# Optimization experiments

Hardware: AMD Instinct MI355X
Metric: run time of the kernel (lower is better)

The kernel has to match this reference:

```python
import jax, jax.numpy as jnp
import numpy as np
import math

B, S, D, H = 4, 2048, 1024, 16
DH = D // H  # 64
DFF = 4 * D
EPS = 1e-5


def layer_norm(x, g, b):
    mu = jnp.mean(x, axis=-1, keepdims=True)
    var = jnp.mean(jnp.square(x - mu), axis=-1, keepdims=True)
    return (x - mu) * jax.lax.rsqrt(var + EPS) * g + b


def apply_rope(xq, xk, freqs_cis):
    # xq, xk: [B, S, H, DH]; freqs_cis: [S, DH//2, 2] (cos, sin)
    cos = freqs_cis[None, :, None, :, 0]  # [1, S, 1, DH//2]
    sin = freqs_cis[None, :, None, :, 1]

    def rot(t):
        tr = t.reshape(*t.shape[:-1], DH // 2, 2)
        t0, t1 = tr[..., 0], tr[..., 1]
        o0 = t0 * cos - t1 * sin
        o1 = t0 * sin + t1 * cos
        return jnp.stack([o0, o1], axis=-1).reshape(t.shape)

    return rot(xq), rot(xk)


def setup_inputs() -> dict:
    key = jax.random.key(0)
    ks = jax.random.split(key, 12)
    x = jax.random.normal(ks[0], (B, S, D), dtype=jnp.float32)
    # rotary frequencies (theta = 10000), stored as (cos, sin)
    inv = 1.0 / (10000.0 ** (np.arange(0, DH, 2, dtype=np.float32) / DH))
    t = np.arange(S, dtype=np.float32)
    ang = np.outer(t, inv)  # [S, DH//2]
    freqs_cis = jnp.asarray(np.stack([np.cos(ang), np.sin(ang)], axis=-1))
    s = 1.0 / math.sqrt(D)
    sf = 1.0 / math.sqrt(DFF)
    return {
        "x": x,
        "freqs_cis": freqs_cis,
        "wq": jax.random.normal(ks[1], (D, D), dtype=jnp.float32) * s,
        "wk": jax.random.normal(ks[2], (D, D), dtype=jnp.float32) * s,
        "wv": jax.random.normal(ks[3], (D, D), dtype=jnp.float32) * s,
        "w_proj": jax.random.normal(ks[4], (D, D), dtype=jnp.float32) * s,
        "b_proj": jnp.zeros((D,), dtype=jnp.float32),
        "w_ff1": jax.random.normal(ks[5], (D, DFF), dtype=jnp.float32) * s,
        "b_ff1": jnp.zeros((DFF,), dtype=jnp.float32),
        "w_ff2": jax.random.normal(ks[6], (DFF, D), dtype=jnp.float32) * sf,
        "b_ff2": jnp.zeros((D,), dtype=jnp.float32),
        "ln1_g": jnp.ones((D,), dtype=jnp.float32),
        "ln1_b": jnp.zeros((D,), dtype=jnp.float32),
        "ln2_g": jnp.ones((D,), dtype=jnp.float32),
        "ln2_b": jnp.zeros((D,), dtype=jnp.float32),
    }


def reference(x, freqs_cis, wq, wk, wv, w_proj, b_proj, w_ff1, b_ff1, w_ff2,
              b_ff2, ln1_g, ln1_b, ln2_g, ln2_b):
    # --- attention block (pre-norm) ---
    h = layer_norm(x, ln1_g, ln1_b)
    xq = (h @ wq).reshape(B, S, H, DH)
    xk = (h @ wk).reshape(B, S, H, DH)
    xv = (h @ wv).reshape(B, S, H, DH)
    xq, xk = apply_rope(xq, xk, freqs_cis)
    # [B, H, S, S]
    att = jnp.einsum("bqhd,bkhd->bhqk", xq, xk) / math.sqrt(DH)
    att = jax.nn.softmax(att, axis=-1)
    out = jnp.einsum("bhqk,bkhd->bqhd", att, xv).reshape(B, S, D)
    x = x + out @ w_proj + b_proj
    # --- feed-forward block (pre-norm, GELU) ---
    h2 = layer_norm(x, ln2_g, ln2_b)
    ff = jax.nn.gelu(h2 @ w_ff1 + b_ff1, approximate=False) @ w_ff2 + b_ff2
    return x + ff
```

## Files before the change

kernel.cpp:

```cpp
#include <hip/hip_runtime.h>
#include <hip/hip_bf16.h>


#define Bb_ 4
#define Ss_ 2048
#define Dd_ 1024
#define Hh_ 16
#define DFF_ 4096

typedef __bf16 bf16x8 __attribute__((ext_vector_type(8)));
typedef float f32x4 __attribute__((ext_vector_type(4)));

static __device__ __forceinline__ unsigned short f2bf(float f) {
  union { float f; unsigned u; } v; v.f = f;
  unsigned r = v.u + 0x7FFF + ((v.u >> 16) & 1);
  return (unsigned short)(r >> 16);
}
static __device__ __forceinline__ float bf2f(unsigned short h) {
  union { unsigned u; float f; } v; v.u = ((unsigned)h) << 16;
  return v.f;
}
static __device__ __forceinline__ unsigned cvt_pk_bf16(float lo, float hi) {
  unsigned r;
  asm("v_cvt_pk_bf16_f32 %0, %1, %2" : "=v"(r) : "v"(lo), "v"(hi));
  return r;
}

static __device__ __forceinline__ void gl16(const unsigned short* g, void* l) {
  __builtin_amdgcn_global_load_lds(
      (const __attribute__((address_space(1))) void*)g,
      (__attribute__((address_space(3))) void*)l, 16, 0, 0);
}

__global__ __launch_bounds__(256) void ln_kernel(
    const float* __restrict__ x, const float* __restrict__ g,
    const float* __restrict__ bb, unsigned short* __restrict__ out)
{
  const int row = blockIdx.x;
  const int t = threadIdx.x;
  const float4 v = reinterpret_cast<const float4*>(x + (size_t)row * Dd_)[t];
  float s = v.x + v.y + v.z + v.w;
  float ss = v.x*v.x + v.y*v.y + v.z*v.z + v.w*v.w;
  #pragma unroll
  for (int o = 32; o; o >>= 1) { s += __shfl_down(s, o); ss += __shfl_down(ss, o); }
  __shared__ float red[8];
  if ((t & 63) == 0) { red[t >> 6] = s; red[4 + (t >> 6)] = ss; }
  __syncthreads();
  s = red[0] + red[1] + red[2] + red[3];
  ss = red[4] + red[5] + red[6] + red[7];
  const float mean = s * (1.f / Dd_);
  const float var = ss * (1.f / Dd_) - mean * mean;
  const float inv = rsqrtf(var + 1e-5f);
  const float4 gv = reinterpret_cast<const float4*>(g)[t];
  const float4 bv = reinterpret_cast<const float4*>(bb)[t];
  ushort4 o4;
  o4.x = f2bf((v.x - mean) * inv * gv.x + bv.x);
  o4.y = f2bf((v.y - mean) * inv * gv.y + bv.y);
  o4.z = f2bf((v.z - mean) * inv * gv.z + bv.z);
  o4.w = f2bf((v.w - mean) * inv * gv.w + bv.w);
  reinterpret_cast<ushort4*>(out + (size_t)row * Dd_)[t] = o4;
}

__global__ __launch_bounds__(256) void tconv_kernel(
    const float* __restrict__ src, unsigned short* __restrict__ dst, int K, int N)
{
  __shared__ float tile[32][33];
  const int bx = blockIdx.x, by = blockIdx.y;
  const int tx = threadIdx.x & 31, ty = threadIdx.x >> 5;
  #pragma unroll
  for (int i = 0; i < 4; i++)
    tile[ty + i * 8][tx] = src[(size_t)(by * 32 + ty + i * 8) * N + bx * 32 + tx];
  __syncthreads();
  #pragma unroll
  for (int i = 0; i < 4; i++)
    dst[(size_t)(bx * 32 + ty + i * 8) * K + by * 32 + tx] = f2bf(tile[tx][ty + i * 8]);
}

__global__ __launch_bounds__(256) void tconv3_kernel(
    const float* __restrict__ s0, const float* __restrict__ s1,
    const float* __restrict__ s2, unsigned short* __restrict__ dst)
{
  __shared__ float tile[32][33];
  const int bx = blockIdx.x, by = blockIdx.y, bz = blockIdx.z;
  const float* src = (bz == 0) ? s0 : (bz == 1) ? s1 : s2;
  unsigned short* d = dst + (size_t)bz * 1024 * 1024;
  const int tx = threadIdx.x & 31, ty = threadIdx.x >> 5;
  #pragma unroll
  for (int i = 0; i < 4; i++)
    tile[ty + i * 8][tx] = src[(size_t)(by * 32 + ty + i * 8) * 1024 + bx * 32 + tx];
  __syncthreads();
  #pragma unroll
  for (int i = 0; i < 4; i++)
    d[(size_t)(bx * 32 + ty + i * 8) * 1024 + by * 32 + tx] = f2bf(tile[tx][ty + i * 8]);
}

template<int MODE>
__global__ __launch_bounds__(256) void gemm_kernel(
    const unsigned short* __restrict__ A,
    const unsigned short* __restrict__ BT,
    int K, int nbn, int N,
    const float* __restrict__ bias,
    const float* __restrict__ resid,
    void* __restrict__ out,
    const float* __restrict__ fcp,
    void* __restrict__ out2)
{
  __shared__ unsigned short As[2][128 * 64];
  __shared__ unsigned short Bs[2][128 * 64];
  const int t = threadIdx.x;

  const int nwg = gridDim.x;
  const int id = blockIdx.x;
  const int sid = (id & 7) * (nwg >> 3) + (id >> 3);
  const int bm = sid / nbn, bn = sid % nbn;

  const int w = t >> 6, lane = t & 63;
  const int lq = lane >> 4, lr = lane & 15;
  const int wm = (w >> 1) * 64, wn = (w & 1) * 64;
  const int srow = t >> 3, sg8 = t & 7;
  const int sw8 = sg8 ^ (srow & 7);

  const unsigned short* ag = A  + (size_t)(bm * 128 + srow) * K + sw8 * 8;
  const unsigned short* bg = BT + (size_t)(bn * 128 + srow) * K + sw8 * 8;

  char* AsB = (char*)As;
  char* BsB = (char*)Bs;
  const int csw = (lr & 7) * 8;
  int aoffB[2], boffB[2];
  aoffB[0] = (wm + lr) * 128 + 2 * ((lq * 8) ^ csw);
  aoffB[1] = (wm + lr) * 128 + 2 * ((32 + lq * 8) ^ csw);
  boffB[0] = (wn + lr) * 128 + 2 * ((lq * 8) ^ csw);
  boffB[1] = (wn + lr) * 128 + 2 * ((32 + lq * 8) ^ csw);
  const int sdstB = (srow * 64 + sg8 * 8) * 2;

  f32x4 acc[4][4] = {};
  const int nt = K >> 6;

#define STAGE7(BUF)                                                          \
  {                                                                          \
    _Pragma("unroll")                                                        \
    for (int i_ = 0; i_ < 4; i_++) {                                         \
      gl16(ag + (size_t)i_ * 32 * K, AsB + (BUF) * 16384 + sdstB + i_ * 4096); \
      gl16(bg + (size_t)i_ * 32 * K, BsB + (BUF) * 16384 + sdstB + i_ * 4096); \
    }                                                                        \
    ag += 64; bg += 64;                                                      \
  }

#define COMPUTE7(BUF)                                                        \
  {                                                                          \
    __builtin_amdgcn_s_setprio(1);                                           \
    _Pragma("unroll")                                                        \
    for (int kc_ = 0; kc_ < 2; kc_++) {                                      \
      bf16x8 af[4], bfr[4];                                                  \
      _Pragma("unroll")                                                      \
      for (int i_ = 0; i_ < 4; i_++) {                                       \
        af[i_]  = *reinterpret_cast<const bf16x8*>(AsB + (BUF) * 16384 + aoffB[kc_] + i_ * 2048); \
        bfr[i_] = *reinterpret_cast<const bf16x8*>(BsB + (BUF) * 16384 + boffB[kc_] + i_ * 2048); \
      }                                                                      \
      _Pragma("unroll")                                                      \
      for (int i_ = 0; i_ < 4; i_++)                                         \
        _Pragma("unroll")                                                    \
        for (int j_ = 0; j_ < 4; j_++)                                       \
          acc[i_][j_] = __builtin_amdgcn_mfma_f32_16x16x32_bf16(af[i_], bfr[j_], acc[i_][j_], 0, 0, 0); \
    }                                                                        \
    __builtin_amdgcn_s_setprio(0);                                           \
  }

  STAGE7(0);
  __syncthreads();
  for (int t0 = 0; t0 < nt; t0 += 2) {
    STAGE7(1);
    COMPUTE7(0);
    __syncthreads();
    if (t0 + 2 < nt) STAGE7(0);
    COMPUTE7(1);
    __syncthreads();
  }
#undef STAGE7
#undef COMPUTE7

  const int growbase = bm * 128 + wm + lq * 4;
  const int gcolbase = bn * 128 + wn + lr;

  if (MODE == 0) {
    if (bn < 16) {
      const float qs = (bn < 8) ? 0.125f * 1.44269504088896f : 1.f;
      const float sgn = (lr & 1) ? 1.f : -1.f;
      #pragma unroll
      for (int j = 0; j < 4; j++) {
        const int col = gcolbase + j * 16;
        const int ip = (col & 63) & ~1;
        #pragma unroll
        for (int i = 0; i < 4; i++) {
          #pragma unroll
          for (int r = 0; r < 4; r++) {
            const int grow = growbase + i * 16 + r;
            const int s = grow & (Ss_ - 1);
            const float2 cs = *reinterpret_cast<const float2*>(fcp + (size_t)s * 64 + ip);
            const float v = acc[i][j][r];
            const float p = __shfl_xor(v, 1);
            const float o = (v * cs.x + sgn * p * cs.y) * qs;
            ((unsigned short*)out)[(size_t)grow * N + col] = f2bf(o);
          }
        }
      }
    } else {
      #pragma unroll
      for (int j = 0; j < 4; j++) {
        const int vcol = gcolbase + j * 16 - 2048;
        const int h = vcol >> 6, d = vcol & 63;
        #pragma unroll
        for (int i = 0; i < 4; i++) {
          const int g0 = growbase + i * 16;
          const int b = g0 >> 11, s0 = g0 & (Ss_ - 1);
          ushort4 o4;
          o4.x = f2bf(acc[i][j][0]);
          o4.y = f2bf(acc[i][j][1]);
          o4.z = f2bf(acc[i][j][2]);
          o4.w = f2bf(acc[i][j][3]);
          unsigned short* vr = (unsigned short*)out2 +
              ((size_t)((b * 16 + h) * 64 + d)) * Ss_ + s0;
          *reinterpret_cast<ushort4*>(vr) = o4;
        }
      }
    }
  } else {
    #pragma unroll
    for (int j = 0; j < 4; j++) {
      const int col = gcolbase + j * 16;
      const float bj = bias[col];
      #pragma unroll
      for (int i = 0; i < 4; i++) {
        #pragma unroll
        for (int r = 0; r < 4; r++) {
          const int grow = growbase + i * 16 + r;
          const float v = acc[i][j][r];
          if (MODE == 1 || MODE == 3) {
            ((float*)out)[(size_t)grow * N + col] = v + bj + resid[(size_t)grow * N + col];
          } else {
            const float u = v + bj;
            const float gel = 0.5f * u * (1.f + erff(u * 0.70710678118654752f));
            ((unsigned short*)out)[(size_t)grow * N + col] = f2bf(gel);
          }
        }
      }
    }
  }
}

__global__ __launch_bounds__(512) void attn_kernel(
    const unsigned short* __restrict__ qkv,
    const unsigned short* __restrict__ vt,
    unsigned short* __restrict__ attout)
{
  __shared__ unsigned short Ks[2][64 * 64];
  __shared__ unsigned short Vs[2][64 * 64];
  __shared__ unsigned short Ps[256 * 64];
  const int qt = blockIdx.x, h = blockIdx.y, b = blockIdx.z;
  const int t = threadIdx.x, w = t >> 6, lane = t & 63;
  const int lq = lane >> 4, lr = lane & 15;
  const int srow = t >> 3, sg8 = t & 7;

  const unsigned short* kg = qkv + (size_t)(b * Ss_) * 3072 + 1024 + h * 64;
  const unsigned short* vg = vt + (size_t)((b * 16 + h) * 64) * Ss_;

  bf16x8 aq[2][2];
  {
    const unsigned short* qg = qkv + (size_t)(b * Ss_ + qt * 256) * 3072 + h * 64;
    #pragma unroll
    for (int mt = 0; mt < 2; mt++)
      #pragma unroll
      for (int kc = 0; kc < 2; kc++)
        aq[mt][kc] = *reinterpret_cast<const bf16x8*>(
            qg + (size_t)(w * 32 + mt * 16 + lr) * 3072 + kc * 32 + lq * 8);
  }

  bf16x8 ones;
  #pragma unroll
  for (int j = 0; j < 8; j++) ones[j] = (__bf16)1.0f;

  f32x4 oacc[2][4] = {};
  f32x4 ssum[2] = {};

  const int g8s = sg8 ^ (srow & 7);

  {
    gl16(kg + (size_t)srow * 3072 + g8s * 8, &Ks[0][srow * 64 + sg8 * 8]);
    gl16(vg + (size_t)srow * Ss_  + g8s * 8, &Vs[0][srow * 64 + sg8 * 8]);
  }
  __syncthreads();

  for (int kt = 0; kt < Ss_ / 64; ++kt) {
    const int cur = kt & 1;
    if (kt < Ss_ / 64 - 1) {
      const int nb = cur ^ 1;
      const size_t ko = (size_t)((kt + 1) * 64);
      gl16(kg + (ko + srow) * 3072 + g8s * 8, &Ks[nb][srow * 64 + sg8 * 8]);
      gl16(vg + (size_t)srow * Ss_ + (kt + 1) * 64 + g8s * 8, &Vs[nb][srow * 64 + sg8 * 8]);
    }

    f32x4 sacc[2][4] = {};
    #pragma unroll
    for (int kc = 0; kc < 2; kc++) {
      const int cofs = kc * 32 + lq * 8;
      const int swz = (lr & 7) * 8;
      bf16x8 kb[4];
      #pragma unroll
      for (int nf = 0; nf < 4; nf++)
        kb[nf] = *reinterpret_cast<const bf16x8*>(&Ks[cur][(nf * 16 + lr) * 64 + (cofs ^ swz)]);
      #pragma unroll
      for (int mt = 0; mt < 2; mt++)
        #pragma unroll
        for (int nf = 0; nf < 4; nf++)
          sacc[mt][nf] = __builtin_amdgcn_mfma_f32_16x16x32_bf16(kb[nf], aq[mt][kc], sacc[mt][nf], 0, 0, 0);
    }

    #pragma unroll
    for (int mt = 0; mt < 2; mt++) {
      const int qrow = w * 32 + mt * 16 + lr;
      char* prow = reinterpret_cast<char*>(Ps) + qrow * 128;
      const int sw = (lr & 7) << 4;
      #pragma unroll
      for (int nf = 0; nf < 4; nf++) {
        const float p0 = __builtin_amdgcn_exp2f(sacc[mt][nf][0]);
        const float p1 = __builtin_amdgcn_exp2f(sacc[mt][nf][1]);
        const float p2 = __builtin_amdgcn_exp2f(sacc[mt][nf][2]);
        const float p3 = __builtin_amdgcn_exp2f(sacc[mt][nf][3]);
        uint2 pw;
        pw.x = cvt_pk_bf16(p0, p1);
        pw.y = cvt_pk_bf16(p2, p3);
        *reinterpret_cast<uint2*>(prow + ((nf * 32 + lq * 8) ^ sw)) = pw;
      }
    }

    #pragma unroll
    for (int kc = 0; kc < 2; kc++) {
      const int cofs = kc * 32 + lq * 8;
      const int swz = (lr & 7) * 8;
      bf16x8 pa[2], vb[4];
      #pragma unroll
      for (int mt = 0; mt < 2; mt++) {
        const int qrow = w * 32 + mt * 16 + lr;
        pa[mt] = *reinterpret_cast<const bf16x8*>(
            reinterpret_cast<const char*>(Ps) + qrow * 128 + ((kc * 64 + lq * 16) ^ ((lr & 7) << 4)));
      }
      #pragma unroll
      for (int mt = 0; mt < 2; mt++)
        ssum[mt] = __builtin_amdgcn_mfma_f32_16x16x32_bf16(pa[mt], ones, ssum[mt], 0, 0, 0);
      #pragma unroll
      for (int nf = 0; nf < 4; nf++)
        vb[nf] = *reinterpret_cast<const bf16x8*>(&Vs[cur][(nf * 16 + lr) * 64 + (cofs ^ swz)]);
      #pragma unroll
      for (int mt = 0; mt < 2; mt++)
        #pragma unroll
        for (int nf = 0; nf < 4; nf++)
          oacc[mt][nf] = __builtin_amdgcn_mfma_f32_16x16x32_bf16(pa[mt], vb[nf], oacc[mt][nf], 0, 0, 0);
    }

    __syncthreads();
  }

  #pragma unroll
  for (int mt = 0; mt < 2; mt++) {
    #pragma unroll
    for (int r = 0; r < 4; r++) {
      const float inv = 1.f / ssum[mt][r];
      const int grow = b * Ss_ + qt * 256 + w * 32 + mt * 16 + lq * 4 + r;
      #pragma unroll
      for (int nf = 0; nf < 4; nf++)
        attout[(size_t)grow * Dd_ + h * 64 + nf * 16 + lr] = f2bf(oacc[mt][nf][r] * inv);
    }
  }
}

extern "C" void kernel_launch(void* const* d_in, const int* in_sizes, int n_in,
                              void* d_out, int out_size, void* d_ws, size_t ws_size,
                              hipStream_t stream) {
  const float* x      = (const float*)d_in[0];
  const float* fc     = (const float*)d_in[1];
  const float* wq     = (const float*)d_in[2];
  const float* wk     = (const float*)d_in[3];
  const float* wv     = (const float*)d_in[4];
  const float* w_proj = (const float*)d_in[5];
  const float* b_proj = (const float*)d_in[6];
  const float* w_ff1  = (const float*)d_in[7];
  const float* b_ff1  = (const float*)d_in[8];
  const float* w_ff2  = (const float*)d_in[9];
  const float* b_ff2  = (const float*)d_in[10];
  const float* ln1_g  = (const float*)d_in[11];
  const float* ln1_b  = (const float*)d_in[12];
  const float* ln2_g  = (const float*)d_in[13];
  const float* ln2_b  = (const float*)d_in[14];

  char* ws = (char*)d_ws;
  unsigned short* hb     = (unsigned short*)(ws);
  unsigned short* wqkvT  = (unsigned short*)(ws + 16777216ull);
  unsigned short* wprojT = (unsigned short*)(ws + 23068672ull);
  unsigned short* wff1T  = (unsigned short*)(ws + 25165824ull);
  unsigned short* wff2T  = (unsigned short*)(ws + 33554432ull);
  float*          x2     = (float*)(ws + 41943040ull);
  unsigned short* vtb    = (unsigned short*)(ws + 41943040ull);
  unsigned short* attoutb= (unsigned short*)(ws + 75497472ull);
  unsigned short* qkvb   = (unsigned short*)(ws + 92274688ull);
  unsigned short* ff1b   = qkvb;

  dim3 blk(256);
  dim3 blk512(512);

  tconv3_kernel<<<dim3(32, 32, 3), blk, 0, stream>>>(wq, wk, wv, wqkvT);
  tconv_kernel<<<dim3(32, 32), blk, 0, stream>>>(w_proj, wprojT, 1024, 1024);
  tconv_kernel<<<dim3(128, 32), blk, 0, stream>>>(w_ff1, wff1T, 1024, 4096);
  tconv_kernel<<<dim3(32, 128), blk, 0, stream>>>(w_ff2, wff2T, 4096, 1024);

  ln_kernel<<<8192, blk, 0, stream>>>(x, ln1_g, ln1_b, hb);
  gemm_kernel<0><<<1536, blk, 0, stream>>>(hb, wqkvT, 1024, 24, 3072, nullptr, nullptr, qkvb, fc, vtb);
  attn_kernel<<<dim3(8, 16, 4), blk512, 0, stream>>>(qkvb, vtb, attoutb);
  gemm_kernel<1><<<512, blk, 0, stream>>>(attoutb, wprojT, 1024, 8, 1024, b_proj, x, x2, nullptr, nullptr);
  ln_kernel<<<8192, blk, 0, stream>>>(x2, ln2_g, ln2_b, hb);
  gemm_kernel<2><<<2048, blk, 0, stream>>>(hb, wff1T, 1024, 32, 4096, b_ff1, nullptr, ff1b, nullptr, nullptr);
  gemm_kernel<3><<<512, blk, 0, stream>>>(ff1b, wff2T, 4096, 8, 1024, b_ff2, x2, (float*)d_out, nullptr, nullptr);
}
```

Baseline: 389.1 us.

## Replace double-buffered GEMM LDS pipeline with single-buffered load-sync-compute loop

The GEMM kernel's two LDS buffers are collapsed into one, cutting shared memory per block from 64KB to 32KB. The main loop now loads a K-tile, synchronizes, computes and synchronizes again. This may let more workgroups share a CU, but global-to-LDS loads no longer overlap MFMA compute within a block, so latency hiding depends on other resident waves.

```diff
diff --git a/kernel.cpp b/kernel.cpp
--- a/kernel.cpp
+++ b/kernel.cpp
@@ -105,8 +105,8 @@
     const float* __restrict__ fcp,
     void* __restrict__ out2)
 {
-  __shared__ unsigned short As[2][128 * 64];
-  __shared__ unsigned short Bs[2][128 * 64];
+  __shared__ unsigned short As[128 * 64];
+  __shared__ unsigned short Bs[128 * 64];
   const int t = threadIdx.x;
 
   const int nwg = gridDim.x;
@@ -136,48 +136,33 @@
   f32x4 acc[4][4] = {};
   const int nt = K >> 6;
 
-#define STAGE7(BUF)                                                          \
-  {                                                                          \
-    _Pragma("unroll")                                                        \
-    for (int i_ = 0; i_ < 4; i_++) {                                         \
-      gl16(ag + (size_t)i_ * 32 * K, AsB + (BUF) * 16384 + sdstB + i_ * 4096); \
-      gl16(bg + (size_t)i_ * 32 * K, BsB + (BUF) * 16384 + sdstB + i_ * 4096); \
-    }                                                                        \
-    ag += 64; bg += 64;                                                      \
-  }
-
-#define COMPUTE7(BUF)                                                        \
-  {                                                                          \
-    __builtin_amdgcn_s_setprio(1);                                           \
-    _Pragma("unroll")                                                        \
-    for (int kc_ = 0; kc_ < 2; kc_++) {                                      \
-      bf16x8 af[4], bfr[4];                                                  \
-      _Pragma("unroll")                                                      \
-      for (int i_ = 0; i_ < 4; i_++) {                                       \
-        af[i_]  = *reinterpret_cast<const bf16x8*>(AsB + (BUF) * 16384 + aoffB[kc_] + i_ * 2048); \
-        bfr[i_] = *reinterpret_cast<const bf16x8*>(BsB + (BUF) * 16384 + boffB[kc_] + i_ * 2048); \
-      }                                                                      \
-      _Pragma("unroll")                                                      \
-      for (int i_ = 0; i_ < 4; i_++)                                         \
-        _Pragma("unroll")                                                    \
-        for (int j_ = 0; j_ < 4; j_++)                                       \
-          acc[i_][j_] = __builtin_amdgcn_mfma_f32_16x16x32_bf16(af[i_], bfr[j_], acc[i_][j_], 0, 0, 0); \
-    }                                                                        \
-    __builtin_amdgcn_s_setprio(0);                                           \
-  }
-
-  STAGE7(0);
-  __syncthreads();
-  for (int t0 = 0; t0 < nt; t0 += 2) {
-    STAGE7(1);
-    COMPUTE7(0);
+  for (int t0 = 0; t0 < nt; ++t0) {
+    #pragma unroll
+    for (int i_ = 0; i_ < 4; i_++) {
+      gl16(ag + (size_t)i_ * 32 * K, AsB + sdstB + i_ * 4096);
+      gl16(bg + (size_t)i_ * 32 * K, BsB + sdstB + i_ * 4096);
+    }
+    ag += 64; bg += 64;
     __syncthreads();
-    if (t0 + 2 < nt) STAGE7(0);
-    COMPUTE7(1);
+
+    __builtin_amdgcn_s_setprio(1);
+    #pragma unroll
+    for (int kc_ = 0; kc_ < 2; kc_++) {
+      bf16x8 af[4], bfr[4];
+      #pragma unroll
+      for (int i_ = 0; i_ < 4; i_++) {
+        af[i_]  = *reinterpret_cast<const bf16x8*>(AsB + aoffB[kc_] + i_ * 2048);
+        bfr[i_] = *reinterpret_cast<const bf16x8*>(BsB + boffB[kc_] + i_ * 2048);
+      }
+      #pragma unroll
+      for (int i_ = 0; i_ < 4; i_++)
+        #pragma unroll
+        for (int j_ = 0; j_ < 4; j_++)
+          acc[i_][j_] = __builtin_amdgcn_mfma_f32_16x16x32_bf16(af[i_], bfr[j_], acc[i_][j_], 0, 0, 0);
+    }
+    __builtin_amdgcn_s_setprio(0);
     __syncthreads();
   }
-#undef STAGE7
-#undef COMPUTE7
 
   const int growbase = bm * 128 + wm + lq * 4;
   const int gcolbase = bn * 128 + wn + lr;
```

After: 386.1 us. No clear change (-0.8%).
